# Optimization experiments

Measured on AMD Instinct MI355X. Metric: run time of the kernel, lower is better.

Reference implementation:

```python
import jax, jax.numpy as jnp
import numpy as np

B, R, L, V, D, P, K = 512, 20, 50, 50000, 64, 2, 10
IN_DIM = 2 * P * D
TAU = 0.5


def _gating(x, w1, w2, b2, bg):
    # sigmoid(xW1^T) + bg * tanh(xW2^T + b2)
    return jax.nn.sigmoid(x @ w1.T) + bg * jnp.tanh(x @ w2.T + b2)


def _coatt_scores(u, i, w, b, M):
    uo = jax.nn.relu(u @ w.T + b)
    io = jax.nn.relu(i @ w.T + b)
    # bilinear scores: U @ M @ I^T
    return jnp.einsum('bud,de,bve->buv', uo, M, io)


def _gumbel_hard(logits, key):
    g = jax.random.gumbel(key, logits.shape, logits.dtype)
    y = jax.nn.softmax((logits + g) / TAU, axis=-1)
    yh = jax.nn.one_hot(jnp.argmax(y, axis=-1), logits.shape[-1], dtype=y.dtype)
    return y + jax.lax.stop_gradient(yh - y)  # straight-through hard one-hot


def _forward(user_reviews, item_reviews, emb, gate_w1, gate_w2, gate_b2, gate_bg,
             ra_w, ra_b, ra_M, wa_w, wa_b, wa_M, fm_v, fm_w, fm_b):
    u_emb = emb[user_reviews]            # [B,R,L,D]
    i_emb = emb[item_reviews]            # [B,R,L,D]
    u_rev = _gating(u_emb.sum(axis=-2), gate_w1, gate_w2, gate_b2, gate_bg)  # [B,R,D]
    i_rev = _gating(i_emb.sum(axis=-2), gate_w1, gate_w2, gate_b2, gate_bg)  # [B,R,D]
    key = jax.random.key(42)
    u_reprs, i_reprs = [], []
    for p in range(P):
        s = _coatt_scores(u_rev, i_rev, ra_w, ra_b, ra_M)     # [B,R,R]
        pr = _gumbel_hard(s.max(axis=-1), jax.random.fold_in(key, 2 * p))
        pc = _gumbel_hard(s.max(axis=-2), jax.random.fold_in(key, 2 * p + 1))
        # hard one-hot pointer 'gather' expressed as weighted sum over review axis
        ur = jnp.einsum('br,brld->bld', pr, u_emb)            # [B,L,D]
        ir = jnp.einsum('br,brld->bld', pc, i_emb)            # [B,L,D]
        sw = _coatt_scores(ur, ir, wa_w, wa_b, wa_M)          # [B,L,L]
        wr = jax.nn.softmax(sw.mean(axis=-1), axis=-1)        # [B,L]
        wc = jax.nn.softmax(sw.mean(axis=-2), axis=-1)        # [B,L]
        u_reprs.append(jnp.einsum('bl,bld->bd', wr, ur))
        i_reprs.append(jnp.einsum('bl,bld->bd', wc, ir))
    x = jnp.concatenate(u_reprs + i_reprs, axis=-1)           # [B, 2*P*D]
    lin = x @ fm_w.T + fm_b                                   # [B,1]
    i1 = x @ fm_v
    i2 = (x * x) @ (fm_v * fm_v)
    pair = jnp.sum(i1 * i1 - i2, axis=-1)                     # [B]
    return (lin[:, 0] + 0.5 * pair)[:, None]                  # [B,1]


def setup_inputs() -> dict:
    key = jax.random.key(0)
    ks = jax.random.split(key, 20)
    return {
        'user_reviews': jax.random.randint(ks[0], (B, R, L), 0, V, dtype=jnp.int32),
        'item_reviews': jax.random.randint(ks[1], (B, R, L), 0, V, dtype=jnp.int32),
        'emb': jax.random.normal(ks[2], (V, D), jnp.float32) * 0.1,
        'gate_w1': jax.random.normal(ks[3], (D, D), jnp.float32) * 0.05,
        'gate_w2': jax.random.normal(ks[4], (D, D), jnp.float32) * 0.05,
        'gate_b2': jax.random.normal(ks[5], (D,), jnp.float32) * 0.05,
        'gate_bg': jax.random.normal(ks[6], (D,), jnp.float32) * 0.05,
        'ra_w': jax.random.normal(ks[7], (D, D), jnp.float32) * 0.05,
        'ra_b': jax.random.normal(ks[8], (D,), jnp.float32) * 0.05,
        'ra_M': jax.random.normal(ks[9], (D, D), jnp.float32) * 0.05,
        'wa_w': jax.random.normal(ks[10], (D, D), jnp.float32) * 0.05,
        'wa_b': jax.random.normal(ks[11], (D,), jnp.float32) * 0.05,
        'wa_M': jax.random.normal(ks[12], (D, D), jnp.float32) * 0.05,
        'fm_v': jax.random.normal(ks[13], (IN_DIM, K), jnp.float32) * 0.05,
        'fm_w': jax.random.normal(ks[14], (1, IN_DIM), jnp.float32) * 0.05,
        'fm_b': jax.random.normal(ks[15], (1,), jnp.float32) * 0.05,
    }


def reference(user_reviews, item_reviews, emb, gate_w1, gate_w2, gate_b2, gate_bg,
              ra_w, ra_b, ra_M, wa_w, wa_b, wa_M, fm_v, fm_w, fm_b):
    return _forward(user_reviews, item_reviews, emb, gate_w1, gate_w2, gate_b2, gate_bg,
                    ra_w, ra_b, ra_M, wa_w, wa_b, wa_M, fm_v, fm_w, fm_b)
```

## Files before the change

kernel.cpp:

```cpp
#include <hip/hip_runtime.h>
#include <stdint.h>
#include <math.h>

#define BB 512
#define RR 20
#define LL 50
#define DD 64
#define PP 2
#define KK 10
#define IN_DIM 256
#define VV 50000

__device__ __forceinline__ uint32_t rotl32(uint32_t v, int d) {
  return (v << d) | (v >> (32 - d));
}

__device__ __forceinline__ void tf2x32(uint32_t k0, uint32_t k1,
                                       uint32_t x0, uint32_t x1,
                                       uint32_t& o0, uint32_t& o1) {
  uint32_t ks0 = k0, ks1 = k1, ks2 = k0 ^ k1 ^ 0x1BD11BDAu;
  x0 += ks0; x1 += ks1;
#define TF_RND(r) { x0 += x1; x1 = rotl32(x1, r); x1 ^= x0; }
  TF_RND(13) TF_RND(15) TF_RND(26) TF_RND(6)
  x0 += ks1; x1 += ks2 + 1u;
  TF_RND(17) TF_RND(29) TF_RND(16) TF_RND(24)
  x0 += ks2; x1 += ks0 + 2u;
  TF_RND(13) TF_RND(15) TF_RND(26) TF_RND(6)
  x0 += ks0; x1 += ks1 + 3u;
  TF_RND(17) TF_RND(29) TF_RND(16) TF_RND(24)
  x0 += ks1; x1 += ks2 + 4u;
  TF_RND(13) TF_RND(15) TF_RND(26) TF_RND(6)
  x0 += ks2; x1 += ks0 + 5u;
#undef TF_RND
  o0 = x0; o1 = x1;
}

__device__ __forceinline__ float wave_sum(float v) {
  for (int off = 32; off; off >>= 1) v += __shfl_xor(v, off, 64);
  return v;
}
__device__ __forceinline__ float wave_max(float v) {
  for (int off = 32; off; off >>= 1) v = fmaxf(v, __shfl_xor(v, off, 64));
  return v;
}

__global__ __launch_bounds__(256) void transpose_w(
    const float* __restrict__ w1, const float* __restrict__ w2,
    const float* __restrict__ ra, const float* __restrict__ wa,
    const float* __restrict__ ma,
    float* __restrict__ w1T, float* __restrict__ w2T,
    float* __restrict__ raT, float* __restrict__ waT,
    float* __restrict__ maT) {
  int i = blockIdx.x * 256 + threadIdx.x;
  if (i < DD * DD) {
    int r = i >> 6, c = i & 63;
    w1T[c * DD + r] = w1[i];
    w2T[c * DD + r] = w2[i];
    raT[c * DD + r] = ra[i];
    waT[c * DD + r] = wa[i];
    maT[c * DD + r] = ma[i];
  }
}

__global__ __launch_bounds__(256) void build_tables(
    const float* __restrict__ emb, const float* __restrict__ waT,
    const float* __restrict__ wa_b, const float* __restrict__ maT,
    float* __restrict__ E1, float* __restrict__ E2) {
  __shared__ float A[DD * 68];
  __shared__ float Bs[DD * 68];
  int tid = threadIdx.x;
  int v0 = blockIdx.x * 64;
  {
    int w = tid >> 4;
    int k0 = (tid & 15) * 4;
    for (int rep = 0; rep < 4; ++rep) {
      int wr = rep * 16 + w;
      int v = v0 + wr;
      float4 e4 = {0.f, 0.f, 0.f, 0.f};
      if (v < VV) e4 = *reinterpret_cast<const float4*>(&emb[(size_t)v * DD + k0]);
      A[(k0 + 0) * 68 + wr] = e4.x;
      A[(k0 + 1) * 68 + wr] = e4.y;
      A[(k0 + 2) * 68 + wr] = e4.z;
      A[(k0 + 3) * 68 + wr] = e4.w;
    }
  }
  for (int i = tid; i < DD * 16; i += 256) {
    int k = i >> 4, c = i & 15;
    *reinterpret_cast<float4*>(&Bs[k * 68 + c * 4]) =
        *reinterpret_cast<const float4*>(&waT[k * DD + c * 4]);
  }
  __syncthreads();
  int wq = tid & 15, dq = tid >> 4;
  float4 bias = *reinterpret_cast<const float4*>(&wa_b[dq * 4]);
  float acc[4][4];
#pragma unroll
  for (int i = 0; i < 4; ++i) {
    acc[i][0] = bias.x; acc[i][1] = bias.y; acc[i][2] = bias.z; acc[i][3] = bias.w;
  }
  for (int k = 0; k < DD; ++k) {
    float4 a4 = *reinterpret_cast<const float4*>(&A[k * 68 + wq * 4]);
    float4 b4 = *reinterpret_cast<const float4*>(&Bs[k * 68 + dq * 4]);
    float av[4] = {a4.x, a4.y, a4.z, a4.w};
    float bv[4] = {b4.x, b4.y, b4.z, b4.w};
#pragma unroll
    for (int i = 0; i < 4; ++i)
#pragma unroll
      for (int j = 0; j < 4; ++j) acc[i][j] += av[i] * bv[j];
  }
#pragma unroll
  for (int i = 0; i < 4; ++i)
#pragma unroll
    for (int j = 0; j < 4; ++j) acc[i][j] = fmaxf(acc[i][j], 0.f);
#pragma unroll
  for (int i = 0; i < 4; ++i) {
    int v = v0 + wq * 4 + i;
    if (v < VV) {
      float4 r = {acc[i][0], acc[i][1], acc[i][2], acc[i][3]};
      *reinterpret_cast<float4*>(&E1[(size_t)v * DD + dq * 4]) = r;
    }
  }
  __syncthreads();
#pragma unroll
  for (int j = 0; j < 4; ++j)
#pragma unroll
    for (int i = 0; i < 4; ++i)
      A[(dq * 4 + j) * 68 + wq * 4 + i] = acc[i][j];
  for (int i = tid; i < DD * 16; i += 256) {
    int k = i >> 4, c = i & 15;
    *reinterpret_cast<float4*>(&Bs[k * 68 + c * 4]) =
        *reinterpret_cast<const float4*>(&maT[k * DD + c * 4]);
  }
  __syncthreads();
  float acc2[4][4];
#pragma unroll
  for (int i = 0; i < 4; ++i)
#pragma unroll
    for (int j = 0; j < 4; ++j) acc2[i][j] = 0.f;
  for (int k = 0; k < DD; ++k) {
    float4 a4 = *reinterpret_cast<const float4*>(&A[k * 68 + wq * 4]);
    float4 b4 = *reinterpret_cast<const float4*>(&Bs[k * 68 + dq * 4]);
    float av[4] = {a4.x, a4.y, a4.z, a4.w};
    float bv[4] = {b4.x, b4.y, b4.z, b4.w};
#pragma unroll
    for (int i = 0; i < 4; ++i)
#pragma unroll
      for (int j = 0; j < 4; ++j) acc2[i][j] += av[i] * bv[j];
  }
#pragma unroll
  for (int i = 0; i < 4; ++i) {
    int v = v0 + wq * 4 + i;
    if (v < VV) {
      float4 r = {acc2[i][0], acc2[i][1], acc2[i][2], acc2[i][3]};
      *reinterpret_cast<float4*>(&E2[(size_t)v * DD + dq * 4]) = r;
    }
  }
}

__global__ __launch_bounds__(256) void embed_gate(
    const int* __restrict__ uidx, const int* __restrict__ iidx,
    const float* __restrict__ emb,
    const float* __restrict__ w1T, const float* __restrict__ w2T,
    const float* __restrict__ b2, const float* __restrict__ bg,
    float* __restrict__ u_rev, float* __restrict__ i_rev) {
  __shared__ int idxs[16 * LL];
  __shared__ float us[16][68];
  int tid = threadIdx.x;
  int isItem = (blockIdx.x >= 640);
  const int* src = isItem ? (iidx + (size_t)(blockIdx.x - 640) * 16 * LL)
                          : (uidx + (size_t)blockIdx.x * 16 * LL);
  for (int i = tid; i < 16 * LL; i += 256) idxs[i] = src[i];
  __syncthreads();
  int w = tid >> 6, lane = tid & 63;
  int grp = lane >> 4, q = lane & 15;
  int revl = w * 4 + grp;
  const int* myidx = idxs + revl * LL;
  float4 acc = {0.f, 0.f, 0.f, 0.f};
  for (int l = 0; l < LL; ++l) {
    int v = myidx[l];
    float4 e4 = *reinterpret_cast<const float4*>(&emb[(size_t)v * DD + q * 4]);
    acc.x += e4.x; acc.y += e4.y; acc.z += e4.z; acc.w += e4.w;
  }
  *reinterpret_cast<float4*>(&us[revl][q * 4]) = acc;
  __syncthreads();
  float4 d1 = {0.f, 0.f, 0.f, 0.f}, d2 = {0.f, 0.f, 0.f, 0.f};
  for (int e = 0; e < DD; ++e) {
    float xv = us[revl][e];
    float4 w1v = *reinterpret_cast<const float4*>(&w1T[e * DD + q * 4]);
    float4 w2v = *reinterpret_cast<const float4*>(&w2T[e * DD + q * 4]);
    d1.x += xv * w1v.x; d1.y += xv * w1v.y; d1.z += xv * w1v.z; d1.w += xv * w1v.w;
    d2.x += xv * w2v.x; d2.y += xv * w2v.y; d2.z += xv * w2v.z; d2.w += xv * w2v.w;
  }
  float4 b2v = *reinterpret_cast<const float4*>(&b2[q * 4]);
  float4 bgv = *reinterpret_cast<const float4*>(&bg[q * 4]);
  float4 val;
  val.x = 1.f / (1.f + expf(-d1.x)) + bgv.x * tanhf(d2.x + b2v.x);
  val.y = 1.f / (1.f + expf(-d1.y)) + bgv.y * tanhf(d2.y + b2v.y);
  val.z = 1.f / (1.f + expf(-d1.z)) + bgv.z * tanhf(d2.z + b2v.z);
  val.w = 1.f / (1.f + expf(-d1.w)) + bgv.w * tanhf(d2.w + b2v.w);
  int gid = blockIdx.x * 16 + revl;
  int t = gid % (BB * RR);
  float* dst = (gid >= BB * RR) ? i_rev : u_rev;
  *reinterpret_cast<float4*>(&dst[(size_t)t * DD + q * 4]) = val;
}

__global__ __launch_bounds__(256) void coatt_rev_sel(
    const float* __restrict__ u_rev, const float* __restrict__ i_rev,
    const float* __restrict__ raT, const float* __restrict__ ra_b,
    const float* __restrict__ ra_M, int* __restrict__ sel) {
  int b = blockIdx.x;
  __shared__ float ur[RR * 65], ir[RR * 65], uo[RR * 65], io[RR * 65], au[RR * 65];
  __shared__ float sc[RR * 21];
  __shared__ float rl[RR], cl[RR];
  __shared__ float gval[4][RR];
  int tid = threadIdx.x;
  for (int i = tid; i < RR * DD; i += 256) {
    int r = i >> 6, d = i & 63;
    ur[r * 65 + d] = u_rev[(size_t)b * RR * DD + i];
    ir[r * 65 + d] = i_rev[(size_t)b * RR * DD + i];
  }
  __syncthreads();
  for (int i = tid; i < RR * DD; i += 256) {
    int u = i >> 6, d = i & 63;
    float bb = ra_b[d];
    float a1 = bb, a2 = bb;
    for (int e = 0; e < DD; ++e) {
      float wv = raT[e * DD + d];
      a1 += ur[u * 65 + e] * wv;
      a2 += ir[u * 65 + e] * wv;
    }
    uo[u * 65 + d] = fmaxf(a1, 0.f);
    io[u * 65 + d] = fmaxf(a2, 0.f);
  }
  __syncthreads();
  for (int i = tid; i < RR * DD; i += 256) {
    int u = i >> 6, e = i & 63;
    float a = 0.f;
    for (int d2 = 0; d2 < DD; ++d2) a += uo[u * 65 + d2] * ra_M[d2 * DD + e];
    au[u * 65 + e] = a;
  }
  __syncthreads();
  for (int i = tid; i < RR * RR; i += 256) {
    int u = i / RR, v = i % RR;
    float a = 0.f;
    for (int e = 0; e < DD; ++e) a += au[u * 65 + e] * io[v * 65 + e];
    sc[u * 21 + v] = a;
  }
  __syncthreads();
  if (tid < RR) {
    float m = -INFINITY;
    for (int v = 0; v < RR; ++v) m = fmaxf(m, sc[tid * 21 + v]);
    rl[tid] = m;
  } else if (tid >= 64 && tid < 64 + RR) {
    int v = tid - 64;
    float m = -INFINITY;
    for (int u = 0; u < RR; ++u) m = fmaxf(m, sc[u * 21 + v]);
    cl[v] = m;
  }
  __syncthreads();
  if (tid < 4 * RR) {
    int n = tid / RR, r = tid % RR;
    uint32_t k0, k1, o0, o1;
    tf2x32(0u, 42u, 0u, (uint32_t)n, k0, k1);
    int e = b * RR + r;
    tf2x32(k0, k1, 0u, (uint32_t)e, o0, o1);
    uint32_t bits = o0 ^ o1;
    float u01 = __uint_as_float((bits >> 9) | 0x3f800000u) - 1.0f;
    const float TINY = 1.1754943508222875e-38f;
    float u = fmaxf(u01 + TINY, TINY);
    float g = -logf(-logf(u));
    gval[n][r] = ((n & 1) ? cl[r] : rl[r]) + g;
  }
  __syncthreads();
  if (tid < 4) {
    float best = -INFINITY; int arg = 0;
    for (int r = 0; r < RR; ++r) {
      float v = gval[tid][r];
      if (v > best) { best = v; arg = r; }
    }
    sel[tid * BB + b] = arg;
  }
}

__global__ __launch_bounds__(256) void word_coatt(
    const int* __restrict__ uidx, const int* __restrict__ iidx,
    const float* __restrict__ emb,
    const float* __restrict__ E1, const float* __restrict__ E2,
    const int* __restrict__ sel, float* __restrict__ x) {
  int bid = blockIdx.x;
  int p = bid >> 9, b = bid & (BB - 1);
  int ru = sel[(2 * p) * BB + b];
  int rv = sel[(2 * p + 1) * BB + b];
  __shared__ int uw[LL], iw[LL];
  __shared__ float E1u[LL * 65], E2i[LL * 65];
  __shared__ float ubar[DD], zbar[DD];
  __shared__ float rm[LL], cm[LL];
  int tid = threadIdx.x;
  if (tid < LL) uw[tid] = uidx[((size_t)b * RR + ru) * LL + tid];
  else if (tid >= 64 && tid < 64 + LL) iw[tid - 64] = iidx[((size_t)b * RR + rv) * LL + (tid - 64)];
  __syncthreads();
  for (int i = tid; i < LL * DD; i += 256) {
    int l = i >> 6, d = i & 63;
    E1u[l * 65 + d] = E1[(size_t)uw[l] * DD + d];
    E2i[l * 65 + d] = E2[(size_t)iw[l] * DD + d];
  }
  __syncthreads();
  if (tid < DD) {
    float s = 0.f;
    for (int l = 0; l < LL; ++l) s += E1u[l * 65 + tid];
    ubar[tid] = s / 50.f;
  } else if (tid < 128) {
    int d = tid - 64;
    float s = 0.f;
    for (int l = 0; l < LL; ++l) s += E2i[l * 65 + d];
    zbar[d] = s / 50.f;
  }
  __syncthreads();
  if (tid < LL) {
    float a = 0.f;
    for (int e = 0; e < DD; ++e) a += E1u[tid * 65 + e] * zbar[e];
    rm[tid] = a;
  } else if (tid >= 64 && tid < 64 + LL) {
    int lj = tid - 64;
    float a = 0.f;
    for (int e = 0; e < DD; ++e) a += ubar[e] * E2i[lj * 65 + e];
    cm[lj] = a;
  }
  __syncthreads();
  int w = tid >> 6, lane = tid & 63;
  if (w == 0) {
    float v = (lane < LL) ? rm[lane] : -INFINITY;
    float m = wave_max(v);
    float ex = (lane < LL) ? expf(rm[lane] - m) : 0.f;
    float sm = wave_sum(ex);
    if (lane < LL) rm[lane] = ex / sm;
  } else if (w == 1) {
    float v = (lane < LL) ? cm[lane] : -INFINITY;
    float m = wave_max(v);
    float ex = (lane < LL) ? expf(cm[lane] - m) : 0.f;
    float sm = wave_sum(ex);
    if (lane < LL) cm[lane] = ex / sm;
  }
  __syncthreads();
  if (w == 0) {
    float a = 0.f;
    for (int l = 0; l < LL; ++l) a += rm[l] * emb[(size_t)uw[l] * DD + lane];
    x[(size_t)b * IN_DIM + p * DD + lane] = a;
  } else if (w == 1) {
    float a = 0.f;
    for (int l = 0; l < LL; ++l) a += cm[l] * emb[(size_t)iw[l] * DD + lane];
    x[(size_t)b * IN_DIM + 2 * DD + p * DD + lane] = a;
  }
}

__global__ __launch_bounds__(256) void fm_head(
    const float* __restrict__ x, const float* __restrict__ fm_v,
    const float* __restrict__ fm_w, const float* __restrict__ fm_b,
    float* __restrict__ out) {
  int tid = threadIdx.x;
  int w = tid >> 6, lane = tid & 63;
  int b = blockIdx.x * 4 + w;
  const float* xb = x + (size_t)b * IN_DIM;
  float4 xv4 = *reinterpret_cast<const float4*>(&xb[lane * 4]);
  float4 wv4 = *reinterpret_cast<const float4*>(&fm_w[lane * 4]);
  float xa[4] = {xv4.x, xv4.y, xv4.z, xv4.w};
  float wa[4] = {wv4.x, wv4.y, wv4.z, wv4.w};
  float lin = 0.f;
  float i1[KK], i2[KK];
#pragma unroll
  for (int k = 0; k < KK; ++k) { i1[k] = 0.f; i2[k] = 0.f; }
#pragma unroll
  for (int jj = 0; jj < 4; ++jj) {
    float xj = xa[jj];
    lin += xj * wa[jj];
    float x2 = xj * xj;
    const float* vr = fm_v + (size_t)(lane * 4 + jj) * KK;
#pragma unroll
    for (int k = 0; k < KK; ++k) {
      float v = vr[k];
      i1[k] += xj * v;
      i2[k] += x2 * (v * v);
    }
  }
  lin = wave_sum(lin);
  float pair = 0.f;
#pragma unroll
  for (int k = 0; k < KK; ++k) {
    float s1 = wave_sum(i1[k]);
    float s2 = wave_sum(i2[k]);
    pair += s1 * s1 - s2;
  }
  if (lane == 0) out[b] = (lin + fm_b[0]) + 0.5f * pair;
}

extern "C" void kernel_launch(void* const* d_in, const int* in_sizes, int n_in,
                              void* d_out, int out_size, void* d_ws, size_t ws_size,
                              hipStream_t stream) {
  (void)in_sizes; (void)n_in; (void)out_size; (void)ws_size;
  const int*   user_reviews = (const int*)d_in[0];
  const int*   item_reviews = (const int*)d_in[1];
  const float* emb  = (const float*)d_in[2];
  const float* gw1  = (const float*)d_in[3];
  const float* gw2  = (const float*)d_in[4];
  const float* gb2  = (const float*)d_in[5];
  const float* gbg  = (const float*)d_in[6];
  const float* ra_w = (const float*)d_in[7];
  const float* ra_b = (const float*)d_in[8];
  const float* ra_M = (const float*)d_in[9];
  const float* wa_w = (const float*)d_in[10];
  const float* wa_b = (const float*)d_in[11];
  const float* wa_M = (const float*)d_in[12];
  const float* fm_v = (const float*)d_in[13];
  const float* fm_w = (const float*)d_in[14];
  const float* fm_b = (const float*)d_in[15];
  float* out = (float*)d_out;

  float* ws = (float*)d_ws;
  float* u_rev = ws;
  float* i_rev = u_rev + BB * RR * DD;
  float* x     = i_rev + BB * RR * DD;
  float* w1T   = x + BB * IN_DIM;
  float* w2T   = w1T + DD * DD;
  float* raT   = w2T + DD * DD;
  float* waT   = raT + DD * DD;
  float* maT   = waT + DD * DD;
  float* E1    = maT + DD * DD;
  float* E2    = E1 + (size_t)VV * DD;
  int*   sel   = (int*)(E2 + (size_t)VV * DD);

  transpose_w<<<dim3(16), dim3(256), 0, stream>>>(gw1, gw2, ra_w, wa_w, wa_M,
                                                  w1T, w2T, raT, waT, maT);
  build_tables<<<dim3((VV + 63) / 64), dim3(256), 0, stream>>>(emb, waT, wa_b, maT, E1, E2);
  embed_gate<<<dim3(1280), dim3(256), 0, stream>>>(
      user_reviews, item_reviews, emb, w1T, w2T, gb2, gbg, u_rev, i_rev);
  coatt_rev_sel<<<dim3(BB), dim3(256), 0, stream>>>(
      u_rev, i_rev, raT, ra_b, ra_M, sel);
  word_coatt<<<dim3(PP * BB), dim3(256), 0, stream>>>(
      user_reviews, item_reviews, emb, E1, E2, sel, x);
  fm_head<<<dim3(128), dim3(256), 0, stream>>>(x, fm_v, fm_w, fm_b, out);
}
```

Measured before the change: 101.5 us.

## Rework thread mappings in build_tables, embed_gate and coatt_rev_sel

build_tables now maps consecutive threads to consecutive vocabulary rows when loading embeddings, which makes the transposed writes into shared memory bank-friendly. embed_gate processes 32 reviews per block with two independent gather chains per thread, giving more memory-level parallelism and half as many blocks. coatt_rev_sel switches its projection matmuls to float4 outputs per thread with a padded row stride of 68, which cuts scalar global weight loads. The cost is higher register use and fewer blocks in embed_gate.

```diff
diff --git a/kernel.cpp b/kernel.cpp
--- a/kernel.cpp
+++ b/kernel.cpp
@@ -71,11 +71,11 @@
   int tid = threadIdx.x;
   int v0 = blockIdx.x * 64;
   {
-    int w = tid >> 4;
-    int k0 = (tid & 15) * 4;
+    int wr = tid & 63;
+    int qk = tid >> 6;
+    int v = v0 + wr;
     for (int rep = 0; rep < 4; ++rep) {
-      int wr = rep * 16 + w;
-      int v = v0 + wr;
+      int k0 = rep * 16 + qk * 4;
       float4 e4 = {0.f, 0.f, 0.f, 0.f};
       if (v < VV) e4 = *reinterpret_cast<const float4*>(&emb[(size_t)v * DD + k0]);
       A[(k0 + 0) * 68 + wr] = e4.x;
@@ -162,45 +162,53 @@
     const float* __restrict__ w1T, const float* __restrict__ w2T,
     const float* __restrict__ b2, const float* __restrict__ bg,
     float* __restrict__ u_rev, float* __restrict__ i_rev) {
-  __shared__ int idxs[16 * LL];
-  __shared__ float us[16][68];
+  __shared__ int idxs[32 * LL];
+  __shared__ float us[32][68];
   int tid = threadIdx.x;
-  int isItem = (blockIdx.x >= 640);
-  const int* src = isItem ? (iidx + (size_t)(blockIdx.x - 640) * 16 * LL)
-                          : (uidx + (size_t)blockIdx.x * 16 * LL);
-  for (int i = tid; i < 16 * LL; i += 256) idxs[i] = src[i];
+  int isItem = (blockIdx.x >= 320);
+  const int* src = isItem ? (iidx + (size_t)(blockIdx.x - 320) * 32 * LL)
+                          : (uidx + (size_t)blockIdx.x * 32 * LL);
+  for (int i = tid; i < 32 * LL; i += 256) idxs[i] = src[i];
   __syncthreads();
   int w = tid >> 6, lane = tid & 63;
   int grp = lane >> 4, q = lane & 15;
-  int revl = w * 4 + grp;
-  const int* myidx = idxs + revl * LL;
-  float4 acc = {0.f, 0.f, 0.f, 0.f};
+  int r0 = w * 8 + grp * 2;
+  const int* i0 = idxs + r0 * LL;
+  const int* i1 = idxs + (r0 + 1) * LL;
+  float4 a0 = {0.f, 0.f, 0.f, 0.f};
+  float4 a1 = {0.f, 0.f, 0.f, 0.f};
+#pragma unroll 5
   for (int l = 0; l < LL; ++l) {
-    int v = myidx[l];
-    float4 e4 = *reinterpret_cast<const float4*>(&emb[(size_t)v * DD + q * 4]);
-    acc.x += e4.x; acc.y += e4.y; acc.z += e4.z; acc.w += e4.w;
-  }
-  *reinterpret_cast<float4*>(&us[revl][q * 4]) = acc;
-  __syncthreads();
-  float4 d1 = {0.f, 0.f, 0.f, 0.f}, d2 = {0.f, 0.f, 0.f, 0.f};
-  for (int e = 0; e < DD; ++e) {
-    float xv = us[revl][e];
-    float4 w1v = *reinterpret_cast<const float4*>(&w1T[e * DD + q * 4]);
-    float4 w2v = *reinterpret_cast<const float4*>(&w2T[e * DD + q * 4]);
-    d1.x += xv * w1v.x; d1.y += xv * w1v.y; d1.z += xv * w1v.z; d1.w += xv * w1v.w;
-    d2.x += xv * w2v.x; d2.y += xv * w2v.y; d2.z += xv * w2v.z; d2.w += xv * w2v.w;
-  }
-  float4 b2v = *reinterpret_cast<const float4*>(&b2[q * 4]);
-  float4 bgv = *reinterpret_cast<const float4*>(&bg[q * 4]);
-  float4 val;
-  val.x = 1.f / (1.f + expf(-d1.x)) + bgv.x * tanhf(d2.x + b2v.x);
-  val.y = 1.f / (1.f + expf(-d1.y)) + bgv.y * tanhf(d2.y + b2v.y);
-  val.z = 1.f / (1.f + expf(-d1.z)) + bgv.z * tanhf(d2.z + b2v.z);
-  val.w = 1.f / (1.f + expf(-d1.w)) + bgv.w * tanhf(d2.w + b2v.w);
-  int gid = blockIdx.x * 16 + revl;
-  int t = gid % (BB * RR);
-  float* dst = (gid >= BB * RR) ? i_rev : u_rev;
-  *reinterpret_cast<float4*>(&dst[(size_t)t * DD + q * 4]) = val;
+    float4 e0 = *reinterpret_cast<const float4*>(&emb[(size_t)i0[l] * DD + q * 4]);
+    float4 e1 = *reinterpret_cast<const float4*>(&emb[(size_t)i1[l] * DD + q * 4]);
+    a0.x += e0.x; a0.y += e0.y; a0.z += e0.z; a0.w += e0.w;
+    a1.x += e1.x; a1.y += e1.y; a1.z += e1.z; a1.w += e1.w;
+  }
+  *reinterpret_cast<float4*>(&us[r0][q * 4]) = a0;
+  *reinterpret_cast<float4*>(&us[r0 + 1][q * 4]) = a1;
+  __syncthreads();
+  for (int rr = 0; rr < 2; ++rr) {
+    int revl = w * 8 + grp * 2 + rr;
+    float4 d1 = {0.f, 0.f, 0.f, 0.f}, d2 = {0.f, 0.f, 0.f, 0.f};
+    for (int e = 0; e < DD; ++e) {
+      float xv = us[revl][e];
+      float4 w1v = *reinterpret_cast<const float4*>(&w1T[e * DD + q * 4]);
+      float4 w2v = *reinterpret_cast<const float4*>(&w2T[e * DD + q * 4]);
+      d1.x += xv * w1v.x; d1.y += xv * w1v.y; d1.z += xv * w1v.z; d1.w += xv * w1v.w;
+      d2.x += xv * w2v.x; d2.y += xv * w2v.y; d2.z += xv * w2v.z; d2.w += xv * w2v.w;
+    }
+    float4 b2v = *reinterpret_cast<const float4*>(&b2[q * 4]);
+    float4 bgv = *reinterpret_cast<const float4*>(&bg[q * 4]);
+    float4 val;
+    val.x = 1.f / (1.f + expf(-d1.x)) + bgv.x * tanhf(d2.x + b2v.x);
+    val.y = 1.f / (1.f + expf(-d1.y)) + bgv.y * tanhf(d2.y + b2v.y);
+    val.z = 1.f / (1.f + expf(-d1.z)) + bgv.z * tanhf(d2.z + b2v.z);
+    val.w = 1.f / (1.f + expf(-d1.w)) + bgv.w * tanhf(d2.w + b2v.w);
+    int gid = blockIdx.x * 32 + revl;
+    int t = gid % (BB * RR);
+    float* dst = (gid >= BB * RR) ? i_rev : u_rev;
+    *reinterpret_cast<float4*>(&dst[(size_t)t * DD + q * 4]) = val;
+  }
 }
 
 __global__ __launch_bounds__(256) void coatt_rev_sel(
@@ -208,41 +216,53 @@
     const float* __restrict__ raT, const float* __restrict__ ra_b,
     const float* __restrict__ ra_M, int* __restrict__ sel) {
   int b = blockIdx.x;
-  __shared__ float ur[RR * 65], ir[RR * 65], uo[RR * 65], io[RR * 65], au[RR * 65];
+  __shared__ float ur[RR * 68], ir[RR * 68], uo[RR * 68], io[RR * 68], au[RR * 68];
   __shared__ float sc[RR * 21];
   __shared__ float rl[RR], cl[RR];
   __shared__ float gval[4][RR];
   int tid = threadIdx.x;
-  for (int i = tid; i < RR * DD; i += 256) {
-    int r = i >> 6, d = i & 63;
-    ur[r * 65 + d] = u_rev[(size_t)b * RR * DD + i];
-    ir[r * 65 + d] = i_rev[(size_t)b * RR * DD + i];
-  }
-  __syncthreads();
-  for (int i = tid; i < RR * DD; i += 256) {
-    int u = i >> 6, d = i & 63;
-    float bb = ra_b[d];
-    float a1 = bb, a2 = bb;
+  for (int i = tid; i < RR * 16; i += 256) {
+    int r = i >> 4, qq = i & 15;
+    *reinterpret_cast<float4*>(&ur[r * 68 + qq * 4]) =
+        *reinterpret_cast<const float4*>(&u_rev[(size_t)b * RR * DD + r * DD + qq * 4]);
+    *reinterpret_cast<float4*>(&ir[r * 68 + qq * 4]) =
+        *reinterpret_cast<const float4*>(&i_rev[(size_t)b * RR * DD + r * DD + qq * 4]);
+  }
+  __syncthreads();
+  for (int s = tid; s < RR * 16; s += 256) {
+    int u = s >> 4, q = s & 15;
+    float4 bias = *reinterpret_cast<const float4*>(&ra_b[q * 4]);
+    float4 a1 = bias, a2 = bias;
     for (int e = 0; e < DD; ++e) {
-      float wv = raT[e * DD + d];
-      a1 += ur[u * 65 + e] * wv;
-      a2 += ir[u * 65 + e] * wv;
-    }
-    uo[u * 65 + d] = fmaxf(a1, 0.f);
-    io[u * 65 + d] = fmaxf(a2, 0.f);
-  }
-  __syncthreads();
-  for (int i = tid; i < RR * DD; i += 256) {
-    int u = i >> 6, e = i & 63;
-    float a = 0.f;
-    for (int d2 = 0; d2 < DD; ++d2) a += uo[u * 65 + d2] * ra_M[d2 * DD + e];
-    au[u * 65 + e] = a;
+      float xu = ur[u * 68 + e];
+      float xi = ir[u * 68 + e];
+      float4 wv = *reinterpret_cast<const float4*>(&raT[e * DD + q * 4]);
+      a1.x += xu * wv.x; a1.y += xu * wv.y; a1.z += xu * wv.z; a1.w += xu * wv.w;
+      a2.x += xi * wv.x; a2.y += xi * wv.y; a2.z += xi * wv.z; a2.w += xi * wv.w;
+    }
+    a1.x = fmaxf(a1.x, 0.f); a1.y = fmaxf(a1.y, 0.f);
+    a1.z = fmaxf(a1.z, 0.f); a1.w = fmaxf(a1.w, 0.f);
+    a2.x = fmaxf(a2.x, 0.f); a2.y = fmaxf(a2.y, 0.f);
+    a2.z = fmaxf(a2.z, 0.f); a2.w = fmaxf(a2.w, 0.f);
+    *reinterpret_cast<float4*>(&uo[u * 68 + q * 4]) = a1;
+    *reinterpret_cast<float4*>(&io[u * 68 + q * 4]) = a2;
+  }
+  __syncthreads();
+  for (int s = tid; s < RR * 16; s += 256) {
+    int u = s >> 4, q = s & 15;
+    float4 a = {0.f, 0.f, 0.f, 0.f};
+    for (int d2 = 0; d2 < DD; ++d2) {
+      float xv = uo[u * 68 + d2];
+      float4 mv = *reinterpret_cast<const float4*>(&ra_M[d2 * DD + q * 4]);
+      a.x += xv * mv.x; a.y += xv * mv.y; a.z += xv * mv.z; a.w += xv * mv.w;
+    }
+    *reinterpret_cast<float4*>(&au[u * 68 + q * 4]) = a;
   }
   __syncthreads();
   for (int i = tid; i < RR * RR; i += 256) {
     int u = i / RR, v = i % RR;
     float a = 0.f;
-    for (int e = 0; e < DD; ++e) a += au[u * 65 + e] * io[v * 65 + e];
+    for (int e = 0; e < DD; ++e) a += au[u * 68 + e] * io[v * 68 + e];
     sc[u * 21 + v] = a;
   }
   __syncthreads();
@@ -430,7 +450,7 @@
   transpose_w<<<dim3(16), dim3(256), 0, stream>>>(gw1, gw2, ra_w, wa_w, wa_M,
                                                   w1T, w2T, raT, waT, maT);
   build_tables<<<dim3((VV + 63) / 64), dim3(256), 0, stream>>>(emb, waT, wa_b, maT, E1, E2);
-  embed_gate<<<dim3(1280), dim3(256), 0, stream>>>(
+  embed_gate<<<dim3(640), dim3(256), 0, stream>>>(
       user_reviews, item_reviews, emb, w1T, w2T, gb2, gbg, u_rev, i_rev);
   coatt_rev_sel<<<dim3(BB), dim3(256), 0, stream>>>(
       u_rev, i_rev, raT, ra_b, ra_M, sel);
```

Result: slower. 131.7 us (+29.8%).
